# Kernel optimization log

Hardware: AMD Instinct MI355X
Metric: run time of the kernel (lower is better)

The kernel has to match this reference:

```python
import jax, jax.numpy as jnp
import numpy as np

VOCAB, EMB, HID, SEQ = 50257, 512, 512, 4096


def setup_inputs() -> dict:
    key = jax.random.key(0)
    k1, k2, k3, k4, k5, k6 = jax.random.split(key, 6)
    s = 1.0 / np.sqrt(HID)
    return {
        "tokens": jax.random.randint(k1, (SEQ,), 0, VOCAB),
        "emb": jax.random.normal(k2, (VOCAB, EMB), jnp.float32) * 0.02,
        "W_ih": jax.random.normal(k3, (4 * HID, EMB), jnp.float32) * s,
        "W_hh": jax.random.normal(k4, (4 * HID, HID), jnp.float32) * s,
        "b_ih": jax.random.normal(k5, (4 * HID,), jnp.float32) * s,
        "b_hh": jax.random.normal(k6, (4 * HID,), jnp.float32) * s,
    }


def reference(tokens, emb, W_ih, W_hh, b_ih, b_hh):
    # gather all embeddings once: [S, E]
    xs = emb[tokens]
    # precompute input-to-gate projections for all steps: [S, 4H]
    gx = xs @ W_ih.T + b_ih + b_hh
    H = W_hh.shape[1]

    def step(carry, gx_t):
        h, c = carry
        gates = gx_t + h @ W_hh.T  # [4H]
        i, f, g, o = jnp.split(gates, 4)
        i = jax.nn.sigmoid(i)
        f = jax.nn.sigmoid(f)
        g = jnp.tanh(g)
        o = jax.nn.sigmoid(o)
        c = f * c + i * g
        h = o * jnp.tanh(c)
        return (h, c), None

    h0 = jnp.zeros((H,), xs.dtype)
    c0 = jnp.zeros((H,), xs.dtype)
    (h, c), _ = jax.lax.scan(step, (h0, c0), gx)
    return (h, c)
```

## Files before the change

kernel.cpp:

```cpp
#include <hip/hip_runtime.h>
#include <hip/hip_bf16.h>

#define SEQ   4096
#define HID   512
#define GDIM  2048
#define NSCAN 64
#define GRID_SCAN 512

#define GX_BYTES   (33554432L)
#define INIT_WORDS 4106

typedef unsigned uint;
typedef uint  v4u __attribute__((ext_vector_type(4)));
typedef _Float16 half2v __attribute__((ext_vector_type(2)));

static __device__ __forceinline__ half2v pack_f16(float a, float b) {
    return __builtin_bit_cast(half2v, __builtin_amdgcn_cvt_pkrtz(a, b));
}

#if __has_builtin(__builtin_amdgcn_fdot2)
#define FDOT2(a,b,c) __builtin_amdgcn_fdot2((a),(b),(c),false)
#else
static __device__ __forceinline__ float FDOT2(half2v a, half2v b, float c) {
    return c + (float)a.x * (float)b.x + (float)a.y * (float)b.y;
}
#endif

__global__ __launch_bounds__(256) void gemm_gx(
    const int*   __restrict__ tokens,
    const float* __restrict__ emb,
    const float* __restrict__ W_ih,
    const float* __restrict__ b_ih,
    const float* __restrict__ b_hh,
    float*       __restrict__ gx,
    int*         __restrict__ initzone)
{
    __shared__ float As[64][33];
    __shared__ float Bs[64][33];
    __shared__ int   tok_s[64];

    const int tid = threadIdx.x;
    const int j0  = blockIdx.x * 64;
    const int t0  = blockIdx.y * 64;

    if (blockIdx.x == 0 && blockIdx.y == 0) {
        for (int i = tid; i < INIT_WORDS; i += 256) initzone[i] = 0;
    }
    if (tid < 64) tok_s[tid] = tokens[t0 + tid];
    __syncthreads();

    const int i  = tid >> 2;
    const int ko = (tid & 3) * 8;
    const int ty = tid >> 4;
    const int tx = tid & 15;

    const long arow = (long)tok_s[i] * HID;
    const long brow = (long)(j0 + i) * HID;

    float acc[4][4] = {};

    for (int k0 = 0; k0 < HID; k0 += 32) {
        float4 a0 = *(const float4*)&emb[arow + k0 + ko];
        float4 a1 = *(const float4*)&emb[arow + k0 + ko + 4];
        float4 b0 = *(const float4*)&W_ih[brow + k0 + ko];
        float4 b1 = *(const float4*)&W_ih[brow + k0 + ko + 4];
        As[i][ko+0]=a0.x; As[i][ko+1]=a0.y; As[i][ko+2]=a0.z; As[i][ko+3]=a0.w;
        As[i][ko+4]=a1.x; As[i][ko+5]=a1.y; As[i][ko+6]=a1.z; As[i][ko+7]=a1.w;
        Bs[i][ko+0]=b0.x; Bs[i][ko+1]=b0.y; Bs[i][ko+2]=b0.z; Bs[i][ko+3]=b0.w;
        Bs[i][ko+4]=b1.x; Bs[i][ko+5]=b1.y; Bs[i][ko+6]=b1.z; Bs[i][ko+7]=b1.w;
        __syncthreads();

        #pragma unroll
        for (int kk = 0; kk < 32; ++kk) {
            float av0 = As[ty*4+0][kk], av1 = As[ty*4+1][kk];
            float av2 = As[ty*4+2][kk], av3 = As[ty*4+3][kk];
            float bv0 = Bs[tx*4+0][kk], bv1 = Bs[tx*4+1][kk];
            float bv2 = Bs[tx*4+2][kk], bv3 = Bs[tx*4+3][kk];
            acc[0][0] += av0*bv0; acc[0][1] += av0*bv1; acc[0][2] += av0*bv2; acc[0][3] += av0*bv3;
            acc[1][0] += av1*bv0; acc[1][1] += av1*bv1; acc[1][2] += av1*bv2; acc[1][3] += av1*bv3;
            acc[2][0] += av2*bv0; acc[2][1] += av2*bv1; acc[2][2] += av2*bv2; acc[2][3] += av2*bv3;
            acc[3][0] += av3*bv0; acc[3][1] += av3*bv1; acc[3][2] += av3*bv2; acc[3][3] += av3*bv3;
        }
        __syncthreads();
    }

    #pragma unroll
    for (int m = 0; m < 4; ++m) {
        const long t = t0 + ty*4 + m;
        #pragma unroll
        for (int n = 0; n < 4; ++n) {
            const int j = j0 + tx*4 + n;
            gx[t*GDIM + j] = acc[m][n] + b_ih[j] + b_hh[j];
        }
    }
}

__global__ __launch_bounds__(256, 2) void lstm_scan(
    const float* __restrict__ gx,
    const float* __restrict__ W_hh,
    unsigned long long* hp2,
    uint*  elect,
    float* out)
{
    __shared__ uint s_part[2];
    __shared__ uint hs16[2][8 * 36];

    const int tid = threadIdx.x;

    uint xcd;
    asm volatile("s_getreg_b32 %0, hwreg(HW_REG_XCC_ID)" : "=s"(xcd));
    xcd &= 7u;
    if (tid == 0) {
        uint* xcnt    = elect;
        uint* winlock = elect + 8;
        uint* winner  = elect + 9;
        uint slot = __hip_atomic_fetch_add(&xcnt[xcd], 1u,
                        __ATOMIC_RELAXED, __HIP_MEMORY_SCOPE_AGENT);
        if (slot == NSCAN - 1) {
            if (__hip_atomic_fetch_add(winlock, 1u,
                    __ATOMIC_ACQ_REL, __HIP_MEMORY_SCOPE_AGENT) == 0)
                __hip_atomic_store(winner, xcd + 1u,
                    __ATOMIC_RELEASE, __HIP_MEMORY_SCOPE_AGENT);
        }
        uint wn;
        while ((wn = __hip_atomic_load(winner,
                    __ATOMIC_ACQUIRE, __HIP_MEMORY_SCOPE_AGENT)) == 0)
            __builtin_amdgcn_s_sleep(2);
        s_part[0] = (wn - 1u == xcd && slot < NSCAN) ? 1u : 0u;
        s_part[1] = slot;
    }
    __syncthreads();
    if (!s_part[0]) return;
    const int w = (int)s_part[1];

    const int wv = tid >> 6;
    const int l  = tid & 63;
    const int r  = l >> 3;
    const int c  = l & 7;
    const int g  = r >> 1;
    const int uu = r & 1;
    const int unit  = w * 8 + wv * 2 + uu;
    const int grow  = g * 512 + unit;
    const int selu  = (l >= 32) ? 1 : 0;
    const int punit = w * 8 + wv * 2 + selu;
    const int cc  = tid >> 5;
    const int pos = tid & 31;

    const long pubw = (long)(w * 4 + wv) * 4 + selu;

    half2v wreg[32];
    {
        const float* wsrc = W_hh + (long)grow * HID + c * 64;
        #pragma unroll
        for (int j = 0; j < 32; ++j) {
            float2 wp = *(const float2*)&wsrc[2 * j];
            wreg[j] = pack_f16(wp.x, wp.y);
        }
    }

    float cstate = 0.0f;
    float gxcur = (c == 0) ? gx[grow] : 0.0f;

    for (int t = 0; t < SEQ; ++t) {
        const int p = t & 1;

        const unsigned long long* src = hp2 + (long)p * 1024 + 2 * tid;
        const uint e16 = (uint)t & 0xFFFFu;
        unsigned long long v;
        uint w0, w1;
        do {
            v  = __hip_atomic_load(src, __ATOMIC_RELAXED, __HIP_MEMORY_SCOPE_AGENT);
            w0 = (uint)v;
            w1 = (uint)(v >> 32);
        } while ((w0 >> 16) != e16 || (w1 >> 16) != e16);

        asm volatile("" ::: "memory");

        hs16[p][cc * 36 + pos] = (w0 & 0xFFFFu) | (w1 << 16);

        float gxn = 0.0f;
        if (c == 0 && t + 1 < SEQ) gxn = gx[(long)(t + 1) * GDIM + grow];

        __syncthreads();

        uint hh[32];
        #pragma unroll
        for (int j = 0; j < 32; j += 4)
            *(v4u*)&hh[j] = *(const v4u*)&hs16[p][c * 36 + j];

        float acc = 0.0f;
        #pragma unroll
        for (int j = 0; j < 32; ++j)
            acc = FDOT2(wreg[j], *(half2v*)&hh[j], acc);

        acc += __shfl_xor(acc, 1, 64);
        acc += __shfl_xor(acc, 2, 64);
        acc += __shfl_xor(acc, 4, 64);

        const float accg = acc + gxcur;
        gxcur = gxn;

        const float gi = __shfl(accg, 8 * (0 + selu), 64);
        const float gf = __shfl(accg, 8 * (2 + selu), 64);
        const float gc = __shfl(accg, 8 * (4 + selu), 64);
        const float go = __shfl(accg, 8 * (6 + selu), 64);

        const float ig = 1.0f / (1.0f + __expf(-gi));
        const float fg = 1.0f / (1.0f + __expf(-gf));
        const float gg = 2.0f / (1.0f + __expf(-2.0f * gc)) - 1.0f;
        const float og = 1.0f / (1.0f + __expf(-go));
        cstate = fg * cstate + ig * gg;
        const float tc = 2.0f / (1.0f + __expf(-2.0f * cstate)) - 1.0f;
        const float hnew = og * tc;

        if ((l & 31) == 0) {
            half2v ph = pack_f16(hnew, hnew);
            const uint hb = (*(uint*)&ph) & 0xFFFFu;
            const uint pw = (((uint)(t + 1) & 0xFFFFu) << 16) | hb;
            uint* dst = (uint*)hp2 + (long)((t + 1) & 1) * 2048 + pubw;
            __hip_atomic_store(dst, pw,
                               __ATOMIC_RELAXED, __HIP_MEMORY_SCOPE_AGENT);
            if (t == SEQ - 1) {
                out[punit]       = hnew;
                out[HID + punit] = cstate;
            }
        }
    }
}

extern "C" void kernel_launch(void* const* d_in, const int* in_sizes, int n_in,
                              void* d_out, int out_size, void* d_ws, size_t ws_size,
                              hipStream_t stream)
{
    const int*   tokens = (const int*)  d_in[0];
    const float* emb    = (const float*)d_in[1];
    const float* W_ih   = (const float*)d_in[2];
    const float* W_hh   = (const float*)d_in[3];
    const float* b_ih   = (const float*)d_in[4];
    const float* b_hh   = (const float*)d_in[5];
    float* out = (float*)d_out;

    char* ws = (char*)d_ws;
    float*              gx    = (float*)ws;
    unsigned long long* hp2   = (unsigned long long*)(ws + GX_BYTES);
    uint*               elect = (uint*)(ws + GX_BYTES + 16384);
    int*                initz = (int*)(ws + GX_BYTES);

    gemm_gx<<<dim3(GDIM / 64, SEQ / 64), 256, 0, stream>>>(
        tokens, emb, W_ih, b_ih, b_hh, gx, initz);

    lstm_scan<<<dim3(GRID_SCAN), 256, 0, stream>>>(gx, W_hh, hp2, elect, out);
}
```

Baseline: 7.667 ms.

## Add fast-path h exchange via sc0 loads/stores with agent-scope fallback buffer

Adds a second h-publication buffer. Each step's h is written both with a plain sc0 store to a fast buffer and with an agent-scope atomic store to a slow buffer. Consumers poll the fast buffer with sc0 dwordx2 loads, which may hit in the XCD-shared L2, since all scan blocks are elected on one XCD. After a capped number of spins a block falls back permanently to the coherent slow buffer. The aim is lower per-step cross-block latency in the serial recurrence, at the cost of a double store and reliance on cache coherence within one XCD.

```diff
diff --git a/kernel.cpp b/kernel.cpp
--- a/kernel.cpp
+++ b/kernel.cpp
@@ -6,12 +6,14 @@
 #define GDIM  2048
 #define NSCAN 64
 #define GRID_SCAN 512
+#define SPIN_CAP 4096
 
 #define GX_BYTES   (33554432L)
-#define INIT_WORDS 4106
+#define INIT_WORDS 8202
 
 typedef unsigned uint;
 typedef uint  v4u __attribute__((ext_vector_type(4)));
+typedef uint  v2u __attribute__((ext_vector_type(2)));
 typedef _Float16 half2v __attribute__((ext_vector_type(2)));
 
 static __device__ __forceinline__ half2v pack_f16(float a, float b) {
@@ -98,7 +100,8 @@
 __global__ __launch_bounds__(256, 2) void lstm_scan(
     const float* __restrict__ gx,
     const float* __restrict__ W_hh,
-    unsigned long long* hp2,
+    unsigned long long* hpF,
+    unsigned long long* hpS,
     uint*  elect,
     float* out)
 {
@@ -160,19 +163,37 @@
 
     float cstate = 0.0f;
     float gxcur = (c == 0) ? gx[grow] : 0.0f;
+    bool slow = false;
 
     for (int t = 0; t < SEQ; ++t) {
         const int p = t & 1;
-
-        const unsigned long long* src = hp2 + (long)p * 1024 + 2 * tid;
         const uint e16 = (uint)t & 0xFFFFu;
-        unsigned long long v;
+
         uint w0, w1;
-        do {
-            v  = __hip_atomic_load(src, __ATOMIC_RELAXED, __HIP_MEMORY_SCOPE_AGENT);
-            w0 = (uint)v;
-            w1 = (uint)(v >> 32);
-        } while ((w0 >> 16) != e16 || (w1 >> 16) != e16);
+        bool got = false;
+        if (!slow) {
+            const unsigned long long* srcF = hpF + (long)p * 1024 + 2 * tid;
+            int spins = 0;
+            for (;;) {
+                v2u pv;
+                asm volatile("global_load_dwordx2 %0, %1, off sc0\n\t"
+                             "s_waitcnt vmcnt(0)"
+                             : "=v"(pv) : "v"(srcF) : "memory");
+                if (((pv.x >> 16) == e16) & ((pv.y >> 16) == e16)) {
+                    w0 = pv.x; w1 = pv.y; got = true; break;
+                }
+                if (++spins == SPIN_CAP) { slow = true; break; }
+            }
+        }
+        if (!got) {
+            const unsigned long long* srcS = hpS + (long)p * 1024 + 2 * tid;
+            unsigned long long v;
+            do {
+                v  = __hip_atomic_load(srcS, __ATOMIC_RELAXED, __HIP_MEMORY_SCOPE_AGENT);
+                w0 = (uint)v;
+                w1 = (uint)(v >> 32);
+            } while ((w0 >> 16) != e16 || (w1 >> 16) != e16);
+        }
 
         asm volatile("" ::: "memory");
 
@@ -217,8 +238,11 @@
             half2v ph = pack_f16(hnew, hnew);
             const uint hb = (*(uint*)&ph) & 0xFFFFu;
             const uint pw = (((uint)(t + 1) & 0xFFFFu) << 16) | hb;
-            uint* dst = (uint*)hp2 + (long)((t + 1) & 1) * 2048 + pubw;
-            __hip_atomic_store(dst, pw,
+            const long poff = (long)((t + 1) & 1) * 2048 + pubw;
+            uint* dstF = (uint*)hpF + poff;
+            asm volatile("global_store_dword %0, %1, off sc0"
+                         :: "v"(dstF), "v"(pw) : "memory");
+            __hip_atomic_store((uint*)hpS + poff, pw,
                                __ATOMIC_RELAXED, __HIP_MEMORY_SCOPE_AGENT);
             if (t == SEQ - 1) {
                 out[punit]       = hnew;
@@ -242,12 +266,13 @@
 
     char* ws = (char*)d_ws;
     float*              gx    = (float*)ws;
-    unsigned long long* hp2   = (unsigned long long*)(ws + GX_BYTES);
-    uint*               elect = (uint*)(ws + GX_BYTES + 16384);
+    unsigned long long* hpF   = (unsigned long long*)(ws + GX_BYTES);
+    unsigned long long* hpS   = (unsigned long long*)(ws + GX_BYTES + 16384);
+    uint*               elect = (uint*)(ws + GX_BYTES + 32768);
     int*                initz = (int*)(ws + GX_BYTES);
 
     gemm_gx<<<dim3(GDIM / 64, SEQ / 64), 256, 0, stream>>>(
         tokens, emb, W_ih, b_ih, b_hh, gx, initz);
 
-    lstm_scan<<<dim3(GRID_SCAN), 256, 0, stream>>>(gx, W_hh, hp2, elect, out);
-}
+    lstm_scan<<<dim3(GRID_SCAN), 256, 0, stream>>>(gx, W_hh, hpF, hpS, elect, out);
+}
```

Result: slower. 23.98 ms (+212.8%).

## Unroll LSTM scan by four with deeper gx prefetch, DPP reductions, split accumulators

Applied to the files above, without the earlier changes.

Unrolls the recurrent scan loop four times and keeps four gx values in registers, so each one is prefetched four steps ahead instead of one and global load latency is hidden. The dot product now uses four independent accumulators to shorten the FDOT2 dependency chain. The first two butterfly reductions use DPP instead of shuffles. __syncthreads is replaced by an explicit lgkmcnt wait plus s_barrier. Together these aim to cut per-step latency on the serial critical path, at the cost of more registers and larger code.

```diff
diff --git a/kernel.cpp b/kernel.cpp
--- a/kernel.cpp
+++ b/kernel.cpp
@@ -94,6 +94,68 @@
         }
     }
 }
+
+
+#define LSTM_STEP(T, GXREG)                                                    \
+  {                                                                            \
+    const int p = (T) & 1;                                                     \
+    const unsigned long long* src = hp2 + (long)p * 1024 + 2 * tid;            \
+    const uint e16 = (uint)(T) & 0xFFFFu;                                      \
+    unsigned long long v; uint w0, w1;                                         \
+    do {                                                                       \
+      v  = __hip_atomic_load(src, __ATOMIC_RELAXED, __HIP_MEMORY_SCOPE_AGENT); \
+      w0 = (uint)v; w1 = (uint)(v >> 32);                                      \
+    } while ((w0 >> 16) != e16 || (w1 >> 16) != e16);                          \
+    asm volatile("" ::: "memory");                                             \
+    hs16[p][cc * 36 + pos] = (w0 & 0xFFFFu) | (w1 << 16);                      \
+    asm volatile("s_waitcnt lgkmcnt(0)" ::: "memory");                         \
+    __builtin_amdgcn_s_barrier();                                              \
+    asm volatile("" ::: "memory");                                             \
+    uint hh[32];                                                               \
+    _Pragma("unroll")                                                          \
+    for (int j = 0; j < 32; j += 4)                                            \
+      *(v4u*)&hh[j] = *(const v4u*)&hs16[p][c * 36 + j];                       \
+    float a0 = 0.f, a1 = 0.f, a2 = 0.f, a3 = 0.f;                              \
+    _Pragma("unroll")                                                          \
+    for (int j = 0; j < 32; j += 4) {                                          \
+      a0 = FDOT2(wreg[j+0], *(half2v*)&hh[j+0], a0);                           \
+      a1 = FDOT2(wreg[j+1], *(half2v*)&hh[j+1], a1);                           \
+      a2 = FDOT2(wreg[j+2], *(half2v*)&hh[j+2], a2);                           \
+      a3 = FDOT2(wreg[j+3], *(half2v*)&hh[j+3], a3);                           \
+    }                                                                          \
+    float acc = (a0 + a1) + (a2 + a3);                                         \
+    acc += __int_as_float(__builtin_amdgcn_update_dpp(                         \
+              0, __float_as_int(acc), 0xB1, 0xF, 0xF, true));       \
+    acc += __int_as_float(__builtin_amdgcn_update_dpp(                         \
+              0, __float_as_int(acc), 0x4E, 0xF, 0xF, true));       \
+    acc += __shfl_xor(acc, 4, 64);                                  \
+    const float accg = acc + (GXREG);                                          \
+    if (c == 0 && (T) + 4 < SEQ)                                               \
+      GXREG = gx[(long)((T) + 4) * GDIM + grow];                               \
+    const float gi = __shfl(accg, 8 * (0 + selu), 64);                         \
+    const float gf = __shfl(accg, 8 * (2 + selu), 64);                         \
+    const float gc = __shfl(accg, 8 * (4 + selu), 64);                         \
+    const float go = __shfl(accg, 8 * (6 + selu), 64);                         \
+    const float ig = 1.0f / (1.0f + __expf(-gi));                              \
+    const float fg = 1.0f / (1.0f + __expf(-gf));                              \
+    const float gg = 2.0f / (1.0f + __expf(-2.0f * gc)) - 1.0f;                \
+    const float og = 1.0f / (1.0f + __expf(-go));                              \
+    cstate = fg * cstate + ig * gg;                                            \
+    const float tc = 2.0f / (1.0f + __expf(-2.0f * cstate)) - 1.0f;            \
+    const float hnew = og * tc;                                                \
+    if ((l & 31) == 0) {                                                       \
+      half2v ph = pack_f16(hnew, hnew);                                        \
+      const uint hb = (*(uint*)&ph) & 0xFFFFu;                                 \
+      const uint pw = (((uint)((T) + 1) & 0xFFFFu) << 16) | hb;                \
+      uint* dst = (uint*)hp2 + (long)(((T) + 1) & 1) * 2048 + pubw;            \
+      __hip_atomic_store(dst, pw,                                              \
+                         __ATOMIC_RELAXED, __HIP_MEMORY_SCOPE_AGENT);          \
+      if ((T) == SEQ - 1) {                                                    \
+        out[punit]       = hnew;                                               \
+        out[HID + punit] = cstate;                                             \
+      }                                                                        \
+    }                                                                          \
+  }
 
 __global__ __launch_bounds__(256, 2) void lstm_scan(
     const float* __restrict__ gx,
@@ -159,72 +221,20 @@
     }
 
     float cstate = 0.0f;
-    float gxcur = (c == 0) ? gx[grow] : 0.0f;
-
-    for (int t = 0; t < SEQ; ++t) {
-        const int p = t & 1;
-
-        const unsigned long long* src = hp2 + (long)p * 1024 + 2 * tid;
-        const uint e16 = (uint)t & 0xFFFFu;
-        unsigned long long v;
-        uint w0, w1;
-        do {
-            v  = __hip_atomic_load(src, __ATOMIC_RELAXED, __HIP_MEMORY_SCOPE_AGENT);
-            w0 = (uint)v;
-            w1 = (uint)(v >> 32);
-        } while ((w0 >> 16) != e16 || (w1 >> 16) != e16);
-
-        asm volatile("" ::: "memory");
-
-        hs16[p][cc * 36 + pos] = (w0 & 0xFFFFu) | (w1 << 16);
-
-        float gxn = 0.0f;
-        if (c == 0 && t + 1 < SEQ) gxn = gx[(long)(t + 1) * GDIM + grow];
-
-        __syncthreads();
-
-        uint hh[32];
-        #pragma unroll
-        for (int j = 0; j < 32; j += 4)
-            *(v4u*)&hh[j] = *(const v4u*)&hs16[p][c * 36 + j];
-
-        float acc = 0.0f;
-        #pragma unroll
-        for (int j = 0; j < 32; ++j)
-            acc = FDOT2(wreg[j], *(half2v*)&hh[j], acc);
-
-        acc += __shfl_xor(acc, 1, 64);
-        acc += __shfl_xor(acc, 2, 64);
-        acc += __shfl_xor(acc, 4, 64);
-
-        const float accg = acc + gxcur;
-        gxcur = gxn;
-
-        const float gi = __shfl(accg, 8 * (0 + selu), 64);
-        const float gf = __shfl(accg, 8 * (2 + selu), 64);
-        const float gc = __shfl(accg, 8 * (4 + selu), 64);
-        const float go = __shfl(accg, 8 * (6 + selu), 64);
-
-        const float ig = 1.0f / (1.0f + __expf(-gi));
-        const float fg = 1.0f / (1.0f + __expf(-gf));
-        const float gg = 2.0f / (1.0f + __expf(-2.0f * gc)) - 1.0f;
-        const float og = 1.0f / (1.0f + __expf(-go));
-        cstate = fg * cstate + ig * gg;
-        const float tc = 2.0f / (1.0f + __expf(-2.0f * cstate)) - 1.0f;
-        const float hnew = og * tc;
-
-        if ((l & 31) == 0) {
-            half2v ph = pack_f16(hnew, hnew);
-            const uint hb = (*(uint*)&ph) & 0xFFFFu;
-            const uint pw = (((uint)(t + 1) & 0xFFFFu) << 16) | hb;
-            uint* dst = (uint*)hp2 + (long)((t + 1) & 1) * 2048 + pubw;
-            __hip_atomic_store(dst, pw,
-                               __ATOMIC_RELAXED, __HIP_MEMORY_SCOPE_AGENT);
-            if (t == SEQ - 1) {
-                out[punit]       = hnew;
-                out[HID + punit] = cstate;
-            }
-        }
+
+    float gxR0 = 0.f, gxR1 = 0.f, gxR2 = 0.f, gxR3 = 0.f;
+    if (c == 0) {
+        gxR0 = gx[grow];
+        gxR1 = gx[(long)1 * GDIM + grow];
+        gxR2 = gx[(long)2 * GDIM + grow];
+        gxR3 = gx[(long)3 * GDIM + grow];
+    }
+
+    for (int t = 0; t < SEQ; t += 4) {
+        LSTM_STEP(t + 0, gxR0);
+        LSTM_STEP(t + 1, gxR1);
+        LSTM_STEP(t + 2, gxR2);
+        LSTM_STEP(t + 3, gxR3);
     }
 }
 
```

Result: slower. 12.12 ms (+58.0%).
